# Performance work log

Hardware: AMD Instinct MI355X
Metric: run time of the kernel (lower is better)

The kernel has to match this reference:

```python
import jax, jax.numpy as jnp
from jax import lax
import numpy as np

BATCH, SEQ_LEN, ENC_IN, C_OUT = 16, 512, 32, 32
N_ORDER = 256           # window_size
MULTISCALE = (1, 2, 4)
MODES = min(32, SEQ_LEN // 2)  # = 32


def make_hippo(N, dt):
    """HiPPO-LegT transition, bilinear (Tustin) discretization, Legendre eval matrix."""
    Q = np.arange(N, dtype=np.float64)
    R = (2 * Q + 1)[:, None]
    j, i = np.meshgrid(Q, Q)
    A = np.where(i < j, -1.0, (-1.0) ** (i - j + 1)) * R
    B = (-1.0) ** Q[:, None] * R                      # [N,1]
    I = np.eye(N)
    M = I - (dt / 2.0) * A
    Ad = np.linalg.solve(M, I + (dt / 2.0) * A)
    Bd = np.linalg.solve(M, dt * B).squeeze(-1)       # [N]
    vals = np.arange(0.0, 1.0, dt)
    x = 1.0 - 2.0 * vals
    P = np.zeros((N, len(vals)))
    P[0] = 1.0
    if N > 1:
        P[1] = x
    for n in range(1, N - 1):
        P[n + 1] = ((2 * n + 1) * x * P[n] - n * P[n - 1]) / (n + 1)
    E = P.T                                           # [len(vals), N]
    return Ad.astype(np.float32), Bd.astype(np.float32), E.astype(np.float32)


def setup_inputs():
    key = jax.random.key(0)
    ks = jax.random.split(key, 12)
    inp = {}
    inp['x_enc'] = jax.random.normal(ks[0], (BATCH, SEQ_LEN, ENC_IN), jnp.float32)
    inp['x_mark_enc'] = jax.random.normal(ks[1], (BATCH, SEQ_LEN, 4), jnp.float32)
    inp['x_dec'] = jax.random.normal(ks[2], (BATCH, SEQ_LEN, ENC_IN), jnp.float32)
    inp['x_mark_dec'] = jax.random.normal(ks[3], (BATCH, SEQ_LEN, 4), jnp.float32)
    inp['affine_weight'] = jnp.ones((1, 1, ENC_IN), jnp.float32)
    inp['affine_bias'] = jnp.zeros((1, 1, ENC_IN), jnp.float32)
    scale = 1.0 / (N_ORDER * N_ORDER)
    for s in range(3):
        inp[f'wr{s}'] = scale * jax.random.uniform(ks[4 + 2 * s], (N_ORDER, N_ORDER, MODES), jnp.float32)
        inp[f'wi{s}'] = scale * jax.random.uniform(ks[5 + 2 * s], (N_ORDER, N_ORDER, MODES), jnp.float32)
    inp['mlp_w'] = 0.1 * jax.random.normal(ks[10], (1, 3), jnp.float32)
    inp['mlp_b'] = jnp.zeros((1,), jnp.float32)
    inp['proj_w'] = 0.02 * jax.random.normal(ks[11], (ENC_IN, C_OUT), jnp.float32)
    inp['proj_b'] = jnp.zeros((C_OUT,), jnp.float32)
    for s, m in enumerate(MULTISCALE):
        A, Bv, E = make_hippo(N_ORDER, 1.0 / SEQ_LEN / m)
        inp[f'A{s}'] = jnp.asarray(A)
        inp[f'Bv{s}'] = jnp.asarray(Bv)
        inp[f'E{s}'] = jnp.asarray(E)
    return inp


def _hippo_scan(x, A, Bv):
    # x: [B, L, C] -> cs: [L, B, C, N]; c_t = A c_{t-1} + B f_t (applied on last dim)
    B_, L, C = x.shape
    c0 = jnp.zeros((B_, C, A.shape[0]), x.dtype)
    At = A.T
    def step(c, f):                      # f: [B, C]
        c = c @ At + f[..., None] * Bv
        return c, c
    _, cs = lax.scan(step, c0, jnp.transpose(x, (1, 0, 2)))
    return cs


def _spectral_conv(xc, wr, wi):
    # xc: [B, C, N, L]; keep first MODES rfft bins, complex channel mix over N, irfft
    L = xc.shape[-1]
    xf = jnp.fft.rfft(xc)                                # [B,C,N,L//2+1] complex64
    W = (wr + 1j * wi).astype(jnp.complex64)             # [N,N,MODES]
    out = jnp.einsum('bjix,iox->bjox', xf[..., :MODES], W)
    out_ft = jnp.pad(out, ((0, 0), (0, 0), (0, 0), (0, L // 2 + 1 - MODES)))
    return jnp.fft.irfft(out_ft, n=L)                    # [B,C,N,L]


def _forward(x_enc, affine_weight, affine_bias, specs, mlp_w, mlp_b, proj_w, proj_b, hippos):
    means = lax.stop_gradient(jnp.mean(x_enc, axis=1, keepdims=True))
    xc = x_enc - means
    stdev = lax.stop_gradient(jnp.sqrt(jnp.var(xc, axis=1, keepdims=True) + 1e-5))
    x = xc / stdev
    x = x * affine_weight + affine_bias                  # [B, L, C]
    pred_len = SEQ_LEN
    decs = []
    for (wr, wi), (A, Bv, E) in zip(specs, hippos):
        # multiscale slice x[:, -m*pred_len:] clips to full seq_len since pred_len==seq_len
        cs = _hippo_scan(x, A, Bv)                       # [L,B,C,N]
        x_in_c = jnp.transpose(cs, (1, 2, 3, 0))         # [B,C,N,L]
        out1 = _spectral_conv(x_in_c, wr, wi)            # [B,C,N,L]
        x_dec_c = out1[..., pred_len - 1]                # [B,C,N]
        dec = x_dec_c @ E[-pred_len:, :].T               # [B,C,pred_len]
        decs.append(dec)
    stacked = jnp.stack(decs, axis=-1)                   # [B,C,P,3]
    y = stacked @ mlp_w[0] + mlp_b[0]                    # Linear(3,1) + squeeze -> [B,C,P]
    y = jnp.transpose(y, (0, 2, 1))                      # [B,P,C]
    y = (y - affine_bias) / (affine_weight + 1e-10)
    y = y * stdev + means
    return y @ proj_w + proj_b                           # OutputBlock: per-step channel projection


def reference(x_enc, x_mark_enc, x_dec, x_mark_dec, affine_weight, affine_bias,
              wr0, wi0, wr1, wi1, wr2, wi2, mlp_w, mlp_b, proj_w, proj_b,
              A0, Bv0, E0, A1, Bv1, E1, A2, Bv2, E2):
    specs = [(wr0, wi0), (wr1, wi1), (wr2, wi2)]
    hippos = [(A0, Bv0, E0), (A1, Bv1, E1), (A2, Bv2, E2)]
    return _forward(x_enc, affine_weight, affine_bias, specs, mlp_w, mlp_b, proj_w, proj_b, hippos)
```

## Files before the change

kernel.cpp:

```cpp
#include <hip/hip_runtime.h>
#include <math.h>

#define SEQ 512
#define NORD 256
#define MODES 32
#define KBIG (NORD*MODES*2)
#define PI_F 3.14159265358979323846f

typedef _Float16 half8 __attribute__((ext_vector_type(8)));
typedef float floatx4 __attribute__((ext_vector_type(4)));


struct GJob {
  const float* A; const float* B; float* C; const float* scale_ptr;
  int M, N, lda, k0, k1, atomic;
};
struct GJobs { GJob j[6]; };

__global__ __launch_bounds__(256) void gemm32_k(GJobs P) {
  GJob jb = P.j[blockIdx.z];
  int col0 = blockIdx.x * 32;
  int row0 = blockIdx.y * 32;
  if (row0 >= jb.M || col0 >= jb.N) return;
  __shared__ float As[64][34];
  __shared__ float Bs[64][36];
  int tid = threadIdx.x;
  int tx = tid & 15, ty = tid >> 4;
  const float* A = jb.A; const float* B = jb.B;
  int M = jb.M, N = jb.N, lda = jb.lda;
  int kcA = (tid & 15) * 4, rA = tid >> 4;
  int ccB = (tid & 7) * 4, kkB = tid >> 3;
  int gr0 = row0 + rA, gr1 = row0 + rA + 16;
  const float4 z4 = make_float4(0.f, 0.f, 0.f, 0.f);
  float4 a0, a1, b0, b1;
  {
    int kb = jb.k0;
    a0 = (gr0 < M) ? *(const float4*)&A[(size_t)gr0 * lda + kb + kcA] : z4;
    a1 = (gr1 < M) ? *(const float4*)&A[(size_t)gr1 * lda + kb + kcA] : z4;
    b0 = *(const float4*)&B[(size_t)(kb + kkB) * N + col0 + ccB];
    b1 = *(const float4*)&B[(size_t)(kb + kkB + 32) * N + col0 + ccB];
  }
  float acc00 = 0.f, acc01 = 0.f, acc10 = 0.f, acc11 = 0.f;
  for (int kb = jb.k0; kb < jb.k1; kb += 64) {
    As[kcA+0][rA] = a0.x; As[kcA+1][rA] = a0.y; As[kcA+2][rA] = a0.z; As[kcA+3][rA] = a0.w;
    As[kcA+0][rA+16] = a1.x; As[kcA+1][rA+16] = a1.y; As[kcA+2][rA+16] = a1.z; As[kcA+3][rA+16] = a1.w;
    *(float4*)&Bs[kkB][ccB] = b0;
    *(float4*)&Bs[kkB+32][ccB] = b1;
    __syncthreads();
    if (kb + 64 < jb.k1) {
      int kn = kb + 64;
      a0 = (gr0 < M) ? *(const float4*)&A[(size_t)gr0 * lda + kn + kcA] : z4;
      a1 = (gr1 < M) ? *(const float4*)&A[(size_t)gr1 * lda + kn + kcA] : z4;
      b0 = *(const float4*)&B[(size_t)(kn + kkB) * N + col0 + ccB];
      b1 = *(const float4*)&B[(size_t)(kn + kkB + 32) * N + col0 + ccB];
    }
    #pragma unroll
    for (int k = 0; k < 64; k++) {
      float2 av = *(float2*)&As[k][ty * 2];
      float2 bv = *(float2*)&Bs[k][tx * 2];
      acc00 += av.x * bv.x; acc01 += av.x * bv.y;
      acc10 += av.y * bv.x; acc11 += av.y * bv.y;
    }
    __syncthreads();
  }
  float sc = jb.scale_ptr ? *jb.scale_ptr : 1.f;
  int gr = row0 + ty * 2, gc = col0 + tx * 2;
  float v00 = acc00 * sc, v01 = acc01 * sc, v10 = acc10 * sc, v11 = acc11 * sc;
  if (jb.atomic) {
    if (gr < M)     { atomicAdd(&jb.C[(size_t)gr * N + gc], v00);     atomicAdd(&jb.C[(size_t)gr * N + gc + 1], v01); }
    if (gr + 1 < M) { atomicAdd(&jb.C[(size_t)(gr+1) * N + gc], v10); atomicAdd(&jb.C[(size_t)(gr+1) * N + gc + 1], v11); }
  } else {
    if (gr < M)     { jb.C[(size_t)gr * N + gc] = v00;     jb.C[(size_t)gr * N + gc + 1] = v01; }
    if (gr + 1 < M) { jb.C[(size_t)(gr+1) * N + gc] = v10; jb.C[(size_t)(gr+1) * N + gc + 1] = v11; }
  }
}


__global__ __launch_bounds__(256) void prep_k(const float* A0, const float* A1, const float* A2,
                                              const float* B0, const float* B1, const float* B2,
                                              const float* E0, const float* E1, const float* E2,
                                              float* R, float* Kry, float* Et, float* Z) {
  long bid = blockIdx.x;
  if (bid < 768) {
    long idx = bid * 256 + threadIdx.x;
    int scl = (int)(idx >> 16);
    int r = (int)(idx & 65535);
    int m = r >> 8, i2 = r & 255;
    const float* A = scl == 0 ? A0 : (scl == 1 ? A1 : A2);
    R[(size_t)scl * 2 * 65536 + (size_t)m * 256 + i2] = A[(size_t)i2 * 256 + m];
  } else if (bid < 2304) {
    long idx = (bid - 768) * 256 + threadIdx.x;
    int scl = (int)(idx / 131072);
    int r = (int)(idx % 131072);
    int p = r >> 8, o = r & 255;
    const float* E; int rows;
    if (scl == 0) { E = E0; rows = 512; }
    else if (scl == 1) { E = E1; rows = 1024; }
    else { E = E2; rows = 2048; }
    int base = rows - 512;
    Et[(size_t)scl * 131072 + (size_t)o * 512 + p] = E[(size_t)(base + p) * 256 + o];
  } else if (bid < 2307) {
    int scl = (int)(bid - 2304);
    const float* B = scl == 0 ? B0 : (scl == 1 ? B1 : B2);
    Kry[(size_t)scl * 512 * 256 + threadIdx.x] = B[threadIdx.x];
  } else {
    long idx = (bid - 2307) * 256 + threadIdx.x;
    if (idx < 655360) Z[idx] = 0.f;
  }
}


__global__ __launch_bounds__(256) void revin_k(const float* __restrict__ x,
                                               const float* __restrict__ aw,
                                               const float* __restrict__ ab,
                                               float* __restrict__ F,
                                               float* __restrict__ stats) {
  int row = blockIdx.x;
  int b = row >> 5, c = row & 31;
  int tid = threadIdx.x;
  const float* xp = x + (size_t)b * SEQ * 32 + c;
  float v0 = xp[(size_t)tid * 32];
  float v1 = xp[(size_t)(tid + 256) * 32];
  float s = v0 + v1, s2 = v0 * v0 + v1 * v1;
  for (int off = 32; off; off >>= 1) {
    s  += __shfl_down(s,  off, 64);
    s2 += __shfl_down(s2, off, 64);
  }
  __shared__ float ws1[4], ws2[4];
  __shared__ float mean_s, istd_s;
  int wid = tid >> 6, lane = tid & 63;
  if (lane == 0) { ws1[wid] = s; ws2[wid] = s2; }
  __syncthreads();
  if (tid == 0) {
    float t1 = ws1[0] + ws1[1] + ws1[2] + ws1[3];
    float t2 = ws2[0] + ws2[1] + ws2[2] + ws2[3];
    float mean = t1 / 512.f;
    float var = t2 / 512.f - mean * mean;
    float sd = sqrtf(var + 1e-5f);
    mean_s = mean; istd_s = 1.f / sd;
    stats[row] = mean; stats[512 + row] = sd;
  }
  __syncthreads();
  float w = aw[c], bb = ab[c];
  float m = mean_s, is = istd_s;
  F[(size_t)row * SEQ + tid]       = (v0 - m) * is * w + bb;
  F[(size_t)row * SEQ + tid + 256] = (v1 - m) * is * w + bb;
}


__global__ __launch_bounds__(256) void qbuildA_k(const float* __restrict__ Kry,
                                                 float2* __restrict__ Pp, int s0) {
  int bg = blockIdx.x;
  int s = s0 + (bg >> 8);
  int r = bg & 255;
  int k = r & 31, c = r >> 5;
  const float* Kry_s = Kry + (size_t)s * 131072;
  float2* P = Pp + (size_t)s * 65536;
  int i = threadIdx.x;
  float ar = 0.f, ai = 0.f;
  const float step = 2.f * PI_F / 512.f;
  int m0 = c * 64;
  for (int mm = 0; mm < 64; mm++) {
    int m = m0 + mm;
    float kap = Kry_s[(size_t)m * 256 + i];
    float sn, cn; __sincosf(step * (float)((k * m) & 511), &sn, &cn);
    ar += kap * cn; ai -= kap * sn;
  }
  P[(size_t)(c * 32 + k) * 256 + i] = make_float2(ar, ai);
}

__global__ __launch_bounds__(256) void qbuildB_k(const float* __restrict__ Kry,
                                                 const float2* __restrict__ Pp,
                                                 _Float16* __restrict__ Qf, int s0) {
  int bg = blockIdx.x;
  int slab = bg >> 8;
  int s = s0 + slab;
  int r = bg & 255;
  int ig = r & 31, c = r >> 5;
  const float* Kry_s = Kry + (size_t)s * 131072;
  const float2* P = Pp + (size_t)s * 65536;
  unsigned int* Qd = (unsigned int*)(Qf + (size_t)slab * 8388608);
  int tid = threadIdx.x;
  int k = tid & 31, il = tid >> 5;
  int i = ig * 8 + il;
  __shared__ __align__(16) unsigned int buf[16 * 256];
  float ar = 0.f, ai = 0.f;
  for (int cp = 0; cp < c; cp++) {
    float2 p = P[(size_t)(cp * 32 + k) * 256 + i];
    ar += p.x; ai += p.y;
  }
  const float step = 2.f * PI_F / 512.f;
  int m0 = c * 64;
  for (int mb = 0; mb < 64; mb += 16) {
    #pragma unroll
    for (int mm = 0; mm < 16; mm++) {
      int m = m0 + mb + mm;
      float kap = Kry_s[(size_t)m * 256 + i];
      float sn, cn; __sincosf(step * (float)((k * m) & 511), &sn, &cn);
      ar += kap * cn; ai -= kap * sn;
      int st = 511 - m;
      float sn2, cn2; __sincosf(step * (float)((k * st) & 511), &sn2, &cn2);
      float qr = ar * cn2 + ai * sn2;
      float qi = ai * cn2 - ar * sn2;
      qr = fminf(fmaxf(qr, -60000.f), 60000.f);
      qi = fminf(fmaxf(qi, -60000.f), 60000.f);
      _Float16 h0 = (_Float16)qr, h1 = (_Float16)qi;
      unsigned short u0, u1;
      __builtin_memcpy(&u0, &h0, 2); __builtin_memcpy(&u1, &h1, 2);
      buf[(st & 15) * 256 + il * 32 + k] = (unsigned int)u0 | ((unsigned int)u1 << 16);
    }
    __syncthreads();
    int st_hi = 511 - (m0 + mb);
    #pragma unroll
    for (int p = 0; p < 4; p++) {
      int idx = p * 256 + tid;
      int rr = idx >> 6, part = idx & 63;
      int st = st_hi - 15 + rr;
      uint4 v = *(uint4*)&buf[(st & 15) * 256 + part * 4];
      *(uint4*)&Qd[(size_t)st * 8192 + (size_t)ig * 256 + part * 4] = v;
    }
    __syncthreads();
  }
}


__global__ __launch_bounds__(256) void wbigT_k(const float* wr0, const float* wi0,
                                               const float* wr1, const float* wi1,
                                               const float* wr2, const float* wi2,
                                               _Float16* __restrict__ Wt, int s0) {
  int bg = blockIdx.x;
  int slab = bg >> 8;
  int s = s0 + slab;
  int r = bg & 255;
  int og = r & 31, iq = r >> 5;
  const float* wr = s == 0 ? wr0 : (s == 1 ? wr1 : wr2);
  const float* wi = s == 0 ? wi0 : (s == 1 ? wi1 : wi2);
  unsigned int* Wd = (unsigned int*)(Wt + (size_t)slab * 4194304);
  int tid = threadIdx.x;
  int ol = tid >> 5, k = tid & 31;
  int o = og * 8 + ol;
  float sn, cn; __sincosf((2.f * PI_F / 512.f) * (float)k, &sn, &cn);
  float g = ((k == 0) ? (1.f / 512.f) : (2.f / 512.f)) * 4096.f;
  float gc = g * cn, gs = g * sn;
  for (int ii = 0; ii < 32; ii++) {
    int i = iq * 32 + ii;
    float a = wr[(size_t)i * 8192 + o * 32 + k];
    float b = wi[(size_t)i * 8192 + o * 32 + k];
    float v0 = gc * a + gs * b;
    float v1 = gs * a - gc * b;
    _Float16 h0 = (_Float16)v0, h1 = (_Float16)v1;
    unsigned short u0, u1;
    __builtin_memcpy(&u0, &h0, 2); __builtin_memcpy(&u1, &h1, 2);
    Wd[(size_t)o * 8192 + (size_t)i * 32 + k] = (unsigned int)u0 | ((unsigned int)u1 << 16);
  }
}


__global__ __launch_bounds__(256) void umfma_k(const _Float16* __restrict__ Qf,
                                               const _Float16* __restrict__ Wt,
                                               float* __restrict__ U, int s0) {
  __shared__ __align__(16) _Float16 Al[8192];
  __shared__ __align__(16) _Float16 Bl[8192];
  int slab = blockIdx.z >> 4;
  int kslab = blockIdx.z & 15;
  int s = s0 + slab;
  const _Float16* Q = Qf + (size_t)slab * 8388608;
  const _Float16* W = Wt + (size_t)slab * 4194304;
  float* Us = U + (size_t)s * 131072;
  int m0 = blockIdx.x * 128;
  int n0 = blockIdx.y * 128;
  int kb0 = kslab * 1024;
  int tid = threadIdx.x;
  int w = tid >> 6, lane = tid & 63;
  int quad = lane >> 4, lm = lane & 15;
  floatx4 acc[4][4];
  #pragma unroll
  for (int a = 0; a < 4; a++)
    #pragma unroll
    for (int b = 0; b < 4; b++) acc[a][b] = (floatx4)(0.f);
  int wm = (w & 1) * 64, wn = (w >> 1) * 64;
  for (int kb = kb0; kb < kb0 + 1024; kb += 64) {
    __syncthreads();
    #pragma unroll
    for (int p = 0; p < 4; p++) {
      int idx = p * 256 + tid;
      int row = idx >> 3, kc = idx & 7;
      int slot = ((kc >> 2) * 8 + (row >> 4)) * 64 + (kc & 3) * 16 + (row & 15);
      *(half8*)&Al[slot * 8] = *(const half8*)&Q[(size_t)(m0 + row) * 16384 + kb + kc * 8];
      *(half8*)&Bl[slot * 8] = *(const half8*)&W[(size_t)(n0 + row) * 16384 + kb + kc * 8];
    }
    __syncthreads();
    #pragma unroll
    for (int ks = 0; ks < 2; ks++) {
      half8 af[4], bf[4];
      #pragma unroll
      for (int t = 0; t < 4; t++) {
        int mt = (wm >> 4) + t;
        af[t] = *(half8*)&Al[((ks * 8 + mt) * 64 + quad * 16 + lm) * 8];
        int nt = (wn >> 4) + t;
        bf[t] = *(half8*)&Bl[((ks * 8 + nt) * 64 + quad * 16 + lm) * 8];
      }
      #pragma unroll
      for (int mi = 0; mi < 4; mi++)
        #pragma unroll
        for (int ni = 0; ni < 4; ni++)
          acc[mi][ni] = __builtin_amdgcn_mfma_f32_16x16x32_f16(af[mi], bf[ni], acc[mi][ni], 0, 0, 0);
    }
  }
  #pragma unroll
  for (int mi = 0; mi < 4; mi++) {
    int gr0 = m0 + wm + mi * 16 + quad * 4;
    #pragma unroll
    for (int ni = 0; ni < 4; ni++) {
      int gc = n0 + wn + ni * 16 + lm;
      #pragma unroll
      for (int r = 0; r < 4; r++)
        atomicAdd(&Us[(size_t)(gr0 + r) * 256 + gc], acc[mi][ni][r] * (1.f / 4096.f));
    }
  }
}


__global__ __launch_bounds__(256) void final_k(const float* __restrict__ y0,
                                               const float* __restrict__ stats,
                                               const float* __restrict__ aw,
                                               const float* __restrict__ ab,
                                               const float* __restrict__ mlp_b,
                                               const float* __restrict__ pw,
                                               const float* __restrict__ pb,
                                               float* __restrict__ out) {
  int b = blockIdx.y;
  int p0 = blockIdx.x * 8;
  int tid = threadIdx.x;
  __shared__ float ys[32 * 8];
  __shared__ float pws[32 * 32];
  for (int t = tid; t < 1024; t += 256) pws[t] = pw[t];
  int c = tid >> 3, pl = tid & 7;
  int row = b * 32 + c;
  float mean = stats[row], sd = stats[512 + row];
  float raw = y0[(size_t)row * 512 + p0 + pl];
  float v = ((raw + mlp_b[0]) - ab[c]) / (aw[c] + 1e-10f) * sd + mean;
  ys[c * 8 + pl] = v;
  __syncthreads();
  int co = tid & 31; int pl2 = tid >> 5;
  float accv = pb[co];
  #pragma unroll
  for (int cc = 0; cc < 32; cc++) accv += ys[cc * 8 + pl2] * pws[cc * 32 + co];
  out[(size_t)b * 512 * 32 + (size_t)(p0 + pl2) * 32 + co] = accv;
}


extern "C" void kernel_launch(void* const* d_in, const int* in_sizes, int n_in,
                              void* d_out, int out_size, void* d_ws, size_t ws_size,
                              hipStream_t stream) {
  const float* x_enc = (const float*)d_in[0];
  const float* aw = (const float*)d_in[4];
  const float* ab = (const float*)d_in[5];
  const float* wr[3] = {(const float*)d_in[6], (const float*)d_in[8], (const float*)d_in[10]};
  const float* wi[3] = {(const float*)d_in[7], (const float*)d_in[9], (const float*)d_in[11]};
  const float* mlp_w = (const float*)d_in[12];
  const float* mlp_b = (const float*)d_in[13];
  const float* proj_w = (const float*)d_in[14];
  const float* proj_b = (const float*)d_in[15];
  const float* Am[3]  = {(const float*)d_in[16], (const float*)d_in[19], (const float*)d_in[22]};
  const float* Bv[3]  = {(const float*)d_in[17], (const float*)d_in[20], (const float*)d_in[23]};
  const float* Em[3]  = {(const float*)d_in[18], (const float*)d_in[21], (const float*)d_in[24]};

  float* w = (float*)d_ws;
  float* F     = w; w += 512 * 512;
  float* stats = w; w += 1024;
  float* Kry   = w; w += 3 * 512 * 256;
  float* R     = w; w += 3 * 2 * 65536;
  float* U     = w; w += 3 * 512 * 256;
  float* Ttot  = w; w += 512 * 512;
  float* Et    = w; w += 3 * 256 * 512;
  float* y0    = w; w += 512 * 512;
  float* Pp    = w; w += 3 * 65536 * 2;
  _Float16* Qf = (_Float16*)w;

  size_t base_bytes = (size_t)((char*)Qf - (char*)d_ws);
  size_t slab_bytes = (size_t)(8388608 + 4194304) * 2;
  int nS = (ws_size >= base_bytes + 3 * slab_bytes) ? 3 : 1;
  _Float16* Wb = Qf + (size_t)nS * 8388608;

  revin_k<<<512, 256, 0, stream>>>(x_enc, aw, ab, F, stats);
  prep_k<<<4867, 256, 0, stream>>>(Am[0], Am[1], Am[2], Bv[0], Bv[1], Bv[2],
                                   Em[0], Em[1], Em[2], R, Kry, Et, U);

  for (int j = 0; j < 9; j++) {
    GJobs P{};
    int M = 1 << j;
    int cur = j & 1;
    int nz = 0;
    for (int s = 0; s < 3; s++) {
      float* Ks = Kry + (size_t)s * 131072;
      float* Rj = R + (size_t)s * 131072 + (size_t)cur * 65536;
      float* Rn = R + (size_t)s * 131072 + (size_t)(1 - cur) * 65536;
      P.j[nz++] = {Ks, Rj, Ks + (size_t)M * 256, nullptr, M, 256, 256, 0, 256, 0};
      if (j < 8) P.j[nz++] = {Rj, Rj, Rn, nullptr, 256, 256, 256, 0, 256, 0};
    }
    gemm32_k<<<dim3(8, 8, nz), 256, 0, stream>>>(P);
  }

  if (nS == 3) {
    qbuildA_k<<<768, 256, 0, stream>>>(Kry, (float2*)Pp, 0);
    qbuildB_k<<<768, 256, 0, stream>>>(Kry, (const float2*)Pp, Qf, 0);
    wbigT_k<<<768, 256, 0, stream>>>(wr[0], wi[0], wr[1], wi[1], wr[2], wi[2], Wb, 0);
    umfma_k<<<dim3(4, 2, 48), 256, 0, stream>>>(Qf, Wb, U, 0);
  } else {
    for (int s = 0; s < 3; s++) {
      qbuildA_k<<<256, 256, 0, stream>>>(Kry, (float2*)Pp, s);
      qbuildB_k<<<256, 256, 0, stream>>>(Kry, (const float2*)Pp, Qf, s);
      wbigT_k<<<256, 256, 0, stream>>>(wr[0], wi[0], wr[1], wi[1], wr[2], wi[2], Wb, s);
      umfma_k<<<dim3(4, 2, 16), 256, 0, stream>>>(Qf, Wb, U, s);
    }
  }

  {
    GJobs P{};
    for (int s = 0; s < 3; s++)
      P.j[s] = {U + (size_t)s * 131072, Et + (size_t)s * 131072, Ttot,
                mlp_w + s, 512, 512, 256, 0, 256, 1};
    gemm32_k<<<dim3(16, 16, 3), 256, 0, stream>>>(P);
  }

  {
    GJobs P{};
    P.j[0] = {F, Ttot, y0, nullptr, 512, 512, 512, 0, 512, 0};
    gemm32_k<<<dim3(16, 16, 1), 256, 0, stream>>>(P);
  }

  final_k<<<dim3(64, 16), 256, 0, stream>>>(y0, stats, aw, ab, mlp_b, proj_w, proj_b,
                                            (float*)d_out);
}
```

Baseline: 373.4 us.

## Pre-swizzle Q and W into MFMA fragment layout and drop LDS staging

The producer kernels qbuildB_k and wbigT_k now write Q and W directly in the 16x16x32 MFMA fragment-tiled order. This lets umfma_k load each lane's half8 operands straight from global memory with register double-buffering, with no shared-memory staging or barriers. The GEMM grid is reshaped into many smaller tiles (32x64 per wave-pair, k-split 16) to give more blocks. The aim is to remove LDS traffic and syncs in the main fp16 GEMM. The cost is more atomic adds on U and less reuse of operands across waves.

Measured after the change: 363.6 us. -2.6%, faster.

```diff
diff --git a/kernel.cpp b/kernel.cpp
--- a/kernel.cpp
+++ b/kernel.cpp
@@ -179,11 +179,11 @@
   int ig = r & 31, c = r >> 5;
   const float* Kry_s = Kry + (size_t)s * 131072;
   const float2* P = Pp + (size_t)s * 65536;
-  unsigned int* Qd = (unsigned int*)(Qf + (size_t)slab * 8388608);
+  uint4* Qd4 = (uint4*)(Qf + (size_t)slab * 8388608);
   int tid = threadIdx.x;
   int k = tid & 31, il = tid >> 5;
   int i = ig * 8 + il;
-  __shared__ __align__(16) unsigned int buf[16 * 256];
+  __shared__ __align__(16) unsigned int buf[16 * 260];
   float ar = 0.f, ai = 0.f;
   for (int cp = 0; cp < c; cp++) {
     float2 p = P[(size_t)(cp * 32 + k) * 256 + i];
@@ -191,6 +191,8 @@
   }
   const float step = 2.f * PI_F / 512.f;
   int m0 = c * 64;
+  int st_low = tid & 15;
+  int part_base = tid >> 4;
   for (int mb = 0; mb < 64; mb += 16) {
     #pragma unroll
     for (int mm = 0; mm < 16; mm++) {
@@ -207,17 +209,20 @@
       _Float16 h0 = (_Float16)qr, h1 = (_Float16)qi;
       unsigned short u0, u1;
       __builtin_memcpy(&u0, &h0, 2); __builtin_memcpy(&u1, &h1, 2);
-      buf[(st & 15) * 256 + il * 32 + k] = (unsigned int)u0 | ((unsigned int)u1 << 16);
+      buf[(st & 15) * 260 + il * 32 + k] = (unsigned int)u0 | ((unsigned int)u1 << 16);
     }
     __syncthreads();
-    int st_hi = 511 - (m0 + mb);
+    int st_base = 496 - m0 - mb;
+    int st = st_base + st_low;
+    size_t rowbase = (size_t)(st >> 4) * 512;
     #pragma unroll
     for (int p = 0; p < 4; p++) {
-      int idx = p * 256 + tid;
-      int rr = idx >> 6, part = idx & 63;
-      int st = st_hi - 15 + rr;
-      uint4 v = *(uint4*)&buf[(st & 15) * 256 + part * 4];
-      *(uint4*)&Qd[(size_t)st * 8192 + (size_t)ig * 256 + part * 4] = v;
+      int part = part_base + p * 16;
+      int ilw = part >> 3, k4 = part & 7;
+      int iw = ig * 8 + ilw;
+      size_t g = (rowbase + (size_t)(iw * 2 + (k4 >> 2))) * 64
+               + (size_t)((k4 & 3) * 16 + st_low);
+      Qd4[g] = *(const uint4*)&buf[st_low * 260 + ilw * 32 + k4 * 4];
     }
     __syncthreads();
   }
@@ -232,7 +237,7 @@
   int slab = bg >> 8;
   int s = s0 + slab;
   int r = bg & 255;
-  int og = r & 31, iq = r >> 5;
+  int og = r >> 3, iq = r & 7;
   const float* wr = s == 0 ? wr0 : (s == 1 ? wr1 : wr2);
   const float* wi = s == 0 ? wi0 : (s == 1 ? wi1 : wi2);
   unsigned int* Wd = (unsigned int*)(Wt + (size_t)slab * 4194304);
@@ -242,6 +247,8 @@
   float sn, cn; __sincosf((2.f * PI_F / 512.f) * (float)k, &sn, &cn);
   float g = ((k == 0) ? (1.f / 512.f) : (2.f / 512.f)) * 4096.f;
   float gc = g * cn, gs = g * sn;
+  size_t obase = (size_t)(o >> 4) * 512;
+  int osub = (((k >> 2) & 3) * 16 + (o & 15)) * 4 + (k & 3);
   for (int ii = 0; ii < 32; ii++) {
     int i = iq * 32 + ii;
     float a = wr[(size_t)i * 8192 + o * 32 + k];
@@ -251,7 +258,7 @@
     _Float16 h0 = (_Float16)v0, h1 = (_Float16)v1;
     unsigned short u0, u1;
     __builtin_memcpy(&u0, &h0, 2); __builtin_memcpy(&u1, &h1, 2);
-    Wd[(size_t)o * 8192 + (size_t)i * 32 + k] = (unsigned int)u0 | ((unsigned int)u1 << 16);
+    Wd[(obase + (size_t)(i * 2 + (k >> 4))) * 256 + osub] = (unsigned int)u0 | ((unsigned int)u1 << 16);
   }
 }
 
@@ -259,63 +266,70 @@
 __global__ __launch_bounds__(256) void umfma_k(const _Float16* __restrict__ Qf,
                                                const _Float16* __restrict__ Wt,
                                                float* __restrict__ U, int s0) {
-  __shared__ __align__(16) _Float16 Al[8192];
-  __shared__ __align__(16) _Float16 Bl[8192];
-  int slab = blockIdx.z >> 4;
-  int kslab = blockIdx.z & 15;
+  int kslab = blockIdx.x;
+  int y = blockIdx.y;
+  int slab = blockIdx.z;
   int s = s0 + slab;
+  int mtile = y >> 1, nh = y & 1;
   const _Float16* Q = Qf + (size_t)slab * 8388608;
   const _Float16* W = Wt + (size_t)slab * 4194304;
   float* Us = U + (size_t)s * 131072;
-  int m0 = blockIdx.x * 128;
-  int n0 = blockIdx.y * 128;
-  int kb0 = kslab * 1024;
   int tid = threadIdx.x;
   int w = tid >> 6, lane = tid & 63;
+  int wm = w >> 1, wn = w & 1;
   int quad = lane >> 4, lm = lane & 15;
-  floatx4 acc[4][4];
+  int mt0 = mtile * 4 + wm * 2;
+  int nt0 = nh * 8 + wn * 4;
+  int kt0 = kslab * 32;
+  const _Float16* qa = Q + (((size_t)mt0 * 512 + (size_t)kt0) * 64 + (size_t)lane) * 8;
+  const _Float16* wb = W + (((size_t)nt0 * 512 + (size_t)kt0) * 64 + (size_t)lane) * 8;
+  floatx4 acc[2][4];
   #pragma unroll
-  for (int a = 0; a < 4; a++)
+  for (int a = 0; a < 2; a++)
     #pragma unroll
     for (int b = 0; b < 4; b++) acc[a][b] = (floatx4)(0.f);
-  int wm = (w & 1) * 64, wn = (w >> 1) * 64;
-  for (int kb = kb0; kb < kb0 + 1024; kb += 64) {
-    __syncthreads();
-    #pragma unroll
-    for (int p = 0; p < 4; p++) {
-      int idx = p * 256 + tid;
-      int row = idx >> 3, kc = idx & 7;
-      int slot = ((kc >> 2) * 8 + (row >> 4)) * 64 + (kc & 3) * 16 + (row & 15);
-      *(half8*)&Al[slot * 8] = *(const half8*)&Q[(size_t)(m0 + row) * 16384 + kb + kc * 8];
-      *(half8*)&Bl[slot * 8] = *(const half8*)&W[(size_t)(n0 + row) * 16384 + kb + kc * 8];
-    }
-    __syncthreads();
-    #pragma unroll
-    for (int ks = 0; ks < 2; ks++) {
-      half8 af[4], bf[4];
-      #pragma unroll
-      for (int t = 0; t < 4; t++) {
-        int mt = (wm >> 4) + t;
-        af[t] = *(half8*)&Al[((ks * 8 + mt) * 64 + quad * 16 + lm) * 8];
-        int nt = (wn >> 4) + t;
-        bf[t] = *(half8*)&Bl[((ks * 8 + nt) * 64 + quad * 16 + lm) * 8];
-      }
-      #pragma unroll
-      for (int mi = 0; mi < 4; mi++)
-        #pragma unroll
-        for (int ni = 0; ni < 4; ni++)
-          acc[mi][ni] = __builtin_amdgcn_mfma_f32_16x16x32_f16(af[mi], bf[ni], acc[mi][ni], 0, 0, 0);
-    }
-  }
+
+#define QA(mi, kk) (*(const half8*)(qa + (size_t)(mi) * 262144 + (size_t)(kk) * 512))
+#define WB(ni, kk) (*(const half8*)(wb + (size_t)(ni) * 262144 + (size_t)(kk) * 512))
+#define MFMA8(A0, A1, B0, B1, B2, B3) \
+  acc[0][0] = __builtin_amdgcn_mfma_f32_16x16x32_f16(A0, B0, acc[0][0], 0, 0, 0); \
+  acc[0][1] = __builtin_amdgcn_mfma_f32_16x16x32_f16(A0, B1, acc[0][1], 0, 0, 0); \
+  acc[0][2] = __builtin_amdgcn_mfma_f32_16x16x32_f16(A0, B2, acc[0][2], 0, 0, 0); \
+  acc[0][3] = __builtin_amdgcn_mfma_f32_16x16x32_f16(A0, B3, acc[0][3], 0, 0, 0); \
+  acc[1][0] = __builtin_amdgcn_mfma_f32_16x16x32_f16(A1, B0, acc[1][0], 0, 0, 0); \
+  acc[1][1] = __builtin_amdgcn_mfma_f32_16x16x32_f16(A1, B1, acc[1][1], 0, 0, 0); \
+  acc[1][2] = __builtin_amdgcn_mfma_f32_16x16x32_f16(A1, B2, acc[1][2], 0, 0, 0); \
+  acc[1][3] = __builtin_amdgcn_mfma_f32_16x16x32_f16(A1, B3, acc[1][3], 0, 0, 0);
+
+  half8 aA0 = QA(0, 0), aA1 = QA(1, 0);
+  half8 bA0 = WB(0, 0), bA1 = WB(1, 0), bA2 = WB(2, 0), bA3 = WB(3, 0);
+  half8 aB0, aB1, bB0, bB1, bB2, bB3;
+  for (int kt = 0; kt < 30; kt += 2) {
+    aB0 = QA(0, kt + 1); aB1 = QA(1, kt + 1);
+    bB0 = WB(0, kt + 1); bB1 = WB(1, kt + 1); bB2 = WB(2, kt + 1); bB3 = WB(3, kt + 1);
+    MFMA8(aA0, aA1, bA0, bA1, bA2, bA3);
+    aA0 = QA(0, kt + 2); aA1 = QA(1, kt + 2);
+    bA0 = WB(0, kt + 2); bA1 = WB(1, kt + 2); bA2 = WB(2, kt + 2); bA3 = WB(3, kt + 2);
+    MFMA8(aB0, aB1, bB0, bB1, bB2, bB3);
+  }
+  aB0 = QA(0, 31); aB1 = QA(1, 31);
+  bB0 = WB(0, 31); bB1 = WB(1, 31); bB2 = WB(2, 31); bB3 = WB(3, 31);
+  MFMA8(aA0, aA1, bA0, bA1, bA2, bA3);
+  MFMA8(aB0, aB1, bB0, bB1, bB2, bB3);
+#undef QA
+#undef WB
+#undef MFMA8
+
+  const float sc = 1.f / 4096.f;
   #pragma unroll
-  for (int mi = 0; mi < 4; mi++) {
-    int gr0 = m0 + wm + mi * 16 + quad * 4;
+  for (int mi = 0; mi < 2; mi++) {
+    int R0 = (mt0 + mi) * 16 + quad * 4;
     #pragma unroll
     for (int ni = 0; ni < 4; ni++) {
-      int gc = n0 + wn + ni * 16 + lm;
+      int gc = (nt0 + ni) * 16 + lm;
       #pragma unroll
-      for (int r = 0; r < 4; r++)
-        atomicAdd(&Us[(size_t)(gr0 + r) * 256 + gc], acc[mi][ni][r] * (1.f / 4096.f));
+      for (int rr2 = 0; rr2 < 4; rr2++)
+        atomicAdd(&Us[(size_t)(R0 + rr2) * 256 + gc], acc[mi][ni][rr2] * sc);
     }
   }
 }
@@ -406,13 +420,13 @@
     qbuildA_k<<<768, 256, 0, stream>>>(Kry, (float2*)Pp, 0);
     qbuildB_k<<<768, 256, 0, stream>>>(Kry, (const float2*)Pp, Qf, 0);
     wbigT_k<<<768, 256, 0, stream>>>(wr[0], wi[0], wr[1], wi[1], wr[2], wi[2], Wb, 0);
-    umfma_k<<<dim3(4, 2, 48), 256, 0, stream>>>(Qf, Wb, U, 0);
+    umfma_k<<<dim3(16, 16, 3), 256, 0, stream>>>(Qf, Wb, U, 0);
   } else {
     for (int s = 0; s < 3; s++) {
       qbuildA_k<<<256, 256, 0, stream>>>(Kry, (float2*)Pp, s);
       qbuildB_k<<<256, 256, 0, stream>>>(Kry, (const float2*)Pp, Qf, s);
       wbigT_k<<<256, 256, 0, stream>>>(wr[0], wi[0], wr[1], wi[1], wr[2], wi[2], Wb, s);
-      umfma_k<<<dim3(4, 2, 16), 256, 0, stream>>>(Qf, Wb, U, s);
+      umfma_k<<<dim3(16, 16, 1), 256, 0, stream>>>(Qf, Wb, U, s);
     }
   }
 
```
